# Kernel optimization log

Measured on AMD Instinct MI355X. Metric: run time of the kernel, lower is better.

Reference implementation:

```python
import jax, jax.numpy as jnp
import numpy as np


def dct_matrix(N: int) -> jnp.ndarray:
    # Orthonormal DCT-II matrix: D[k, n] = s_k * cos(pi*(2n+1)k / (2N))
    n = jnp.arange(N, dtype=jnp.float32)
    k = jnp.arange(N, dtype=jnp.float32)[:, None]
    D = jnp.cos(jnp.pi * (2.0 * n + 1.0) * k / (2.0 * N))
    scale = jnp.where(k == 0, jnp.sqrt(1.0 / N), jnp.sqrt(2.0 / N))
    return D * scale


def setup_inputs() -> dict:
    key = jax.random.key(0)
    k1, k2, k3 = jax.random.split(key, 3)
    B, C, H, W = 16, 128, 128, 128
    top_k, red = 16, 4
    x = jax.random.normal(k1, (B, C, H, W), dtype=jnp.float32)
    w1 = jax.random.normal(k2, (top_k, top_k // red), dtype=jnp.float32) * (1.0 / np.sqrt(top_k))
    b1 = jnp.zeros((top_k // red,), dtype=jnp.float32)
    w2 = jax.random.normal(k3, (top_k // red, 1), dtype=jnp.float32) * (1.0 / np.sqrt(top_k // red))
    b2 = jnp.zeros((1,), dtype=jnp.float32)
    return {"x": x, "w1": w1, "b1": b1, "w2": w2, "b2": b2}


def reference(x, w1, b1, w2, b2):
    B, C, H, W = x.shape
    top_k = w1.shape[0]
    # dct_energy uses x.detach() in the original -> no grad through this path
    xs = jax.lax.stop_gradient(x)
    DH = dct_matrix(H)
    DW = dct_matrix(W)
    # 2D orthonormal DCT-II via two matmuls: DH @ x @ DW^T
    t = jnp.einsum('hH,bcHW->bchW', DH, xs)
    dct2 = jnp.einsum('bchW,wW->bchw', t, DW)
    energy = jnp.abs(dct2).mean(axis=1).reshape(B, H * W)  # [B, H*W]
    topk_vals, _ = jax.lax.top_k(energy, top_k)  # [B, top_k], descending
    h = jax.nn.relu(topk_vals @ w1 + b1)
    att = jax.nn.sigmoid(h @ w2 + b2)  # [B, 1]
    return x * att[:, :, None, None]
```

## Files before the change

### kernel.cpp

```cpp
#include <hip/hip_runtime.h>


typedef __attribute__((ext_vector_type(8))) _Float16 half8;
typedef __attribute__((ext_vector_type(16))) float f32x16;

#define NCH 32
#define CPB 4

#define Z16 {0.f,0.f,0.f,0.f,0.f,0.f,0.f,0.f,0.f,0.f,0.f,0.f,0.f,0.f,0.f,0.f}

#define SWZ(row, c) (((((row) * 128 + (c)) * 2)) ^ (((row) & 7) << 4))

__device__ __forceinline__ unsigned short f2h(float f) {
    union { _Float16 h; unsigned short u; } cv;
    cv.h = (_Float16)f;
    return cv.u;
}
__device__ __forceinline__ unsigned int pack2(float a, float b) {
    return (unsigned int)f2h(a) | ((unsigned int)f2h(b) << 16);
}

__global__ __launch_bounds__(256) void dct_prep(unsigned short* __restrict__ Dp) {
    int i = blockIdx.x * 256 + threadIdx.x;
    int j = i & 7, r = (i >> 3) & 127, hi = (i >> 10) & 1, kk = i >> 11;
    int c = kk * 16 + hi * 8 + j;
    float s = (r == 0) ? 0.08838834764831845f : 0.125f;
    float ang = (float)((2 * c + 1) * r) * 0.012271846303085130f;
    Dp[i] = f2h(s * cosf(ang));
}

__global__ __launch_bounds__(512) void dct_energy_kernel(
    const float* __restrict__ x, const unsigned short* __restrict__ Dp,
    float* __restrict__ energy, float* __restrict__ partial)
{
    __shared__ __attribute__((aligned(16))) unsigned short Xs[128 * 128];
    __shared__ __attribute__((aligned(16))) unsigned short Ps[128 * 128];

    const int b = blockIdx.x;
    const int chunk = blockIdx.y;
    const int tid = threadIdx.x;
    const int lane = tid & 63;
    const int wid = tid >> 6;
    const int wm = wid >> 1;
    const int wn = wid & 1;
    const int l31 = lane & 31;
    const int hi = lane >> 5;

    const float4* xb4 = (const float4*)(x + (((size_t)(b * 128 + chunk * CPB)) << 14));

    float en0[16], en1[16];
#pragma unroll
    for (int r = 0; r < 16; ++r) { en0[r] = 0.f; en1[r] = 0.f; }

    const int rowX = 32 * wm + l31;
    const int k2a = 64 * wn + l31;
    const unsigned short* dB0 = Dp + k2a * 8;
    const unsigned short* dB1 = Dp + (k2a + 32) * 8;
    const unsigned short* dA  = Dp + rowX * 8;

    float4 ld[8];
#pragma unroll
    for (int i = 0; i < 8; ++i) ld[i] = xb4[i * 512 + tid];
#pragma unroll
    for (int i = 0; i < 8; ++i) {
        int fidx = i * 512 + tid;
        int row = fidx >> 5, c = (fidx & 31) << 2;
        uint2 v; v.x = pack2(ld[i].x, ld[i].y); v.y = pack2(ld[i].z, ld[i].w);
        *(uint2*)((char*)Xs + SWZ(row, c)) = v;
    }
    __syncthreads();

    for (int s = 0; s < CPB; ++s) {
        if (s + 1 < CPB) {
            const float4* nx = xb4 + ((size_t)(s + 1) << 12);
#pragma unroll
            for (int i = 0; i < 8; ++i) ld[i] = nx[i * 512 + tid];
        }

        f32x16 acc0 = Z16, acc1 = Z16;
#pragma unroll
        for (int kk = 0; kk < 8; ++kk) {
            int c0 = kk * 16 + hi * 8;
            int kb = (kk * 2 + hi) << 10;
            half8 aX = *(const half8*)((const char*)Xs + SWZ(rowX, c0));
            half8 bD0 = *(const half8*)(const void*)(dB0 + kb);
            half8 bD1 = *(const half8*)(const void*)(dB1 + kb);
            acc0 = __builtin_amdgcn_mfma_f32_32x32x16_f16(aX, bD0, acc0, 0, 0, 0);
            acc1 = __builtin_amdgcn_mfma_f32_32x32x16_f16(aX, bD1, acc1, 0, 0, 0);
        }
#pragma unroll
        for (int g = 0; g < 4; ++g) {
            int h0 = 32 * wm + 8 * g + 4 * hi;
            uint2 v0; v0.x = pack2(acc0[4 * g + 0], acc0[4 * g + 1]);
            v0.y = pack2(acc0[4 * g + 2], acc0[4 * g + 3]);
            *(uint2*)((char*)Ps + SWZ(k2a, h0)) = v0;
            uint2 v1; v1.x = pack2(acc1[4 * g + 0], acc1[4 * g + 1]);
            v1.y = pack2(acc1[4 * g + 2], acc1[4 * g + 3]);
            *(uint2*)((char*)Ps + SWZ(k2a + 32, h0)) = v1;
        }
        __syncthreads();

        f32x16 d0 = Z16, d1 = Z16;
#pragma unroll
        for (int kk = 0; kk < 8; ++kk) {
            int c0 = kk * 16 + hi * 8;
            int kb = (kk * 2 + hi) << 10;
            half8 aD = *(const half8*)(const void*)(dA + kb);
            half8 bP0 = *(const half8*)((const char*)Ps + SWZ(k2a, c0));
            half8 bP1 = *(const half8*)((const char*)Ps + SWZ(k2a + 32, c0));
            d0 = __builtin_amdgcn_mfma_f32_32x32x16_f16(aD, bP0, d0, 0, 0, 0);
            d1 = __builtin_amdgcn_mfma_f32_32x32x16_f16(aD, bP1, d1, 0, 0, 0);
        }
#pragma unroll
        for (int r = 0; r < 16; ++r) { en0[r] += fabsf(d0[r]); en1[r] += fabsf(d1[r]); }

        if (s + 1 < CPB) {
#pragma unroll
            for (int i = 0; i < 8; ++i) {
                int fidx = i * 512 + tid;
                int row = fidx >> 5, c = (fidx & 31) << 2;
                uint2 v; v.x = pack2(ld[i].x, ld[i].y); v.y = pack2(ld[i].z, ld[i].w);
                *(uint2*)((char*)Xs + SWZ(row, c)) = v;
            }
        }
        __syncthreads();
    }

    if (partial) {
        float* pb = partial + (((size_t)(b * NCH + chunk)) << 14);
#pragma unroll
        for (int r = 0; r < 16; ++r) {
            int row = 32 * wm + (r & 3) + 8 * (r >> 2) + 4 * hi;
            int idx = row * 128 + k2a;
            pb[idx] = en0[r];
            pb[idx + 32] = en1[r];
        }
    } else {
        float* eb = energy + ((size_t)b << 14);
#pragma unroll
        for (int r = 0; r < 16; ++r) {
            int row = 32 * wm + (r & 3) + 8 * (r >> 2) + 4 * hi;
            int idx = row * 128 + k2a;
            atomicAdd(&eb[idx], en0[r]);
            atomicAdd(&eb[idx + 32], en1[r]);
        }
    }
}

__global__ __launch_bounds__(256) void reduce_energy(
    const float* __restrict__ partial, float* __restrict__ energy)
{
    int g = blockIdx.x * 256 + threadIdx.x;
    int b = g >> 14, i = g & 16383;
    const float* p = partial + (((size_t)b * NCH) << 14) + i;
    float s = 0.f;
#pragma unroll
    for (int ch = 0; ch < NCH; ++ch) s += p[(size_t)ch << 14];
    energy[g] = s;
}

__global__ __launch_bounds__(1024) void topk_mlp(
    const float* __restrict__ energy,
    const float* __restrict__ w1, const float* __restrict__ b1,
    const float* __restrict__ w2, const float* __restrict__ b2,
    float* __restrict__ att)
{
    __shared__ float wv[16];
    __shared__ int   wi[16];
    __shared__ float winv_s;
    __shared__ int   wini_s;
    __shared__ float topv[16];
    int b = blockIdx.x, t = threadIdx.x;
    int lane = t & 63, wid = t >> 6;
    const float* eb = energy + ((size_t)b << 14);

    float v[16];
#pragma unroll
    for (int k = 0; k < 16; ++k) v[k] = eb[k * 1024 + t];
    unsigned mask = 0xFFFFu;

    for (int j = 0; j < 16; ++j) {
        float mv = -1e30f; int mi = 0;
#pragma unroll
        for (int k = 0; k < 16; ++k) {
            if ((mask >> k) & 1u) {
                float c = v[k];
                if (c > mv) { mv = c; mi = k * 1024 + t; }
            }
        }
#pragma unroll
        for (int off = 32; off >= 1; off >>= 1) {
            float ov = __shfl_down(mv, off);
            int   oi = __shfl_down(mi, off);
            if (ov > mv) { mv = ov; mi = oi; }
        }
        if (lane == 0) { wv[wid] = mv; wi[wid] = mi; }
        __syncthreads();
        if (t == 0) {
            float bv = wv[0]; int bi = wi[0];
#pragma unroll
            for (int w = 1; w < 16; ++w)
                if (wv[w] > bv) { bv = wv[w]; bi = wi[w]; }
            winv_s = bv; wini_s = bi;
            topv[j] = bv * (1.0f / 128.0f);
        }
        __syncthreads();
        int gw = wini_s;
        if (t == (gw & 1023)) mask &= ~(1u << (gw >> 10));
    }

    if (t == 0) {
        float z = b2[0];
#pragma unroll
        for (int jj = 0; jj < 4; ++jj) {
            float a = b1[jj];
#pragma unroll
            for (int i = 0; i < 16; ++i) a += topv[i] * w1[i * 4 + jj];
            a = fmaxf(a, 0.0f);
            z += a * w2[jj];
        }
        att[b] = 1.0f / (1.0f + expf(-z));
    }
}

__global__ __launch_bounds__(256) void scale_kernel(
    const float4* __restrict__ x4, const float* __restrict__ att,
    float4* __restrict__ out4, int n4)
{
    int i = blockIdx.x * 256 + threadIdx.x;
    int stride = gridDim.x * 256;
    for (; i < n4; i += stride) {
        float a = att[i >> 19];
        float4 v = x4[i];
        v.x *= a; v.y *= a; v.z *= a; v.w *= a;
        out4[i] = v;
    }
}

extern "C" void kernel_launch(void* const* d_in, const int* in_sizes, int n_in,
                              void* d_out, int out_size, void* d_ws, size_t ws_size,
                              hipStream_t stream) {
    const float* x  = (const float*)d_in[0];
    const float* w1 = (const float*)d_in[1];
    const float* b1 = (const float*)d_in[2];
    const float* w2 = (const float*)d_in[3];
    const float* b2 = (const float*)d_in[4];

    char* wsb = (char*)d_ws;
    unsigned short* Dp = (unsigned short*)wsb;
    float* energy = (float*)(wsb + (1 << 15));
    float* att    = (float*)(wsb + (1 << 15) + (1 << 20));
    float* partial = (float*)(wsb + (1 << 21));
    size_t need_partial = (size_t)(1 << 21) + (size_t)16 * NCH * 16384 * 4;
    bool use_partial = (ws_size >= need_partial);

    dct_prep<<<64, 256, 0, stream>>>(Dp);
    if (!use_partial) hipMemsetAsync(energy, 0, (size_t)16 * 16384 * 4, stream);

    dim3 g2(16, NCH);
    dct_energy_kernel<<<g2, 512, 0, stream>>>(x, Dp, energy,
                                              use_partial ? partial : (float*)nullptr);
    if (use_partial) reduce_energy<<<1024, 256, 0, stream>>>(partial, energy);

    topk_mlp<<<16, 1024, 0, stream>>>(energy, w1, b1, w2, b2, att);
    scale_kernel<<<2048, 256, 0, stream>>>((const float4*)x, att,
                                           (float4*)d_out, out_size / 4);
}
```

Before: 318.3 us.

## Split fused DCT energy kernel into two passes via fp16 intermediate in output buffer

Splits the fused two-stage DCT kernel into two kernels. Pass1 runs one block per (batch, channel) and writes the fp16 row-transformed result to global memory, reusing the output buffer as scratch. Pass2 reads that intermediate directly from global memory for the column transform and accumulates absolute energy across 4 channels per block. This raises parallelism in the first stage (2048 blocks instead of 512) and frees LDS, at the cost of an extra write and read of a 64MB fp16 intermediate.

```diff
diff --git a/kernel.cpp b/kernel.cpp
--- a/kernel.cpp
+++ b/kernel.cpp
@@ -5,7 +5,7 @@
 typedef __attribute__((ext_vector_type(16))) float f32x16;
 
 #define NCH 32
-#define CPB 4
+#define CPB2 4
 
 #define Z16 {0.f,0.f,0.f,0.f,0.f,0.f,0.f,0.f,0.f,0.f,0.f,0.f,0.f,0.f,0.f,0.f}
 
@@ -29,13 +29,78 @@
     Dp[i] = f2h(s * cosf(ang));
 }
 
-__global__ __launch_bounds__(512) void dct_energy_kernel(
+__global__ __launch_bounds__(512) void dct_pass1(
     const float* __restrict__ x, const unsigned short* __restrict__ Dp,
+    unsigned short* __restrict__ PG)
+{
+    __shared__ __attribute__((aligned(16))) unsigned short Xs[128 * 128];
+
+    const int b = blockIdx.x;
+    const int c = blockIdx.y;
+    const int tid = threadIdx.x;
+    const int lane = tid & 63;
+    const int wid = tid >> 6;
+    const int wm = wid >> 1;
+    const int wn = wid & 1;
+    const int l31 = lane & 31;
+    const int hi = lane >> 5;
+
+    const float4* xb4 = (const float4*)(x + (((size_t)(b * 128 + c)) << 14));
+
+#pragma unroll
+    for (int i = 0; i < 8; ++i) {
+        float4 v = xb4[i * 512 + tid];
+        int fidx = i * 512 + tid;
+        int row = fidx >> 5, cc = (fidx & 31) << 2;
+        uint2 u; u.x = pack2(v.x, v.y); u.y = pack2(v.z, v.w);
+        *(uint2*)((char*)Xs + SWZ(row, cc)) = u;
+    }
+    __syncthreads();
+
+    const int rowX = 32 * wm + l31;
+    const int k2a = 64 * wn + l31;
+    const unsigned short* dB0 = Dp + k2a * 8;
+    const unsigned short* dB1 = Dp + (k2a + 32) * 8;
+
+    f32x16 acc0 = Z16, acc1 = Z16;
+#pragma unroll
+    for (int kk = 0; kk < 8; ++kk) {
+        int c0 = kk * 16 + hi * 8;
+        int kb = (kk * 2 + hi) << 10;
+        half8 aX = *(const half8*)((const char*)Xs + SWZ(rowX, c0));
+        half8 bD0 = *(const half8*)(const void*)(dB0 + kb);
+        half8 bD1 = *(const half8*)(const void*)(dB1 + kb);
+        acc0 = __builtin_amdgcn_mfma_f32_32x32x16_f16(aX, bD0, acc0, 0, 0, 0);
+        acc1 = __builtin_amdgcn_mfma_f32_32x32x16_f16(aX, bD1, acc1, 0, 0, 0);
+    }
+    __syncthreads();
+
+#pragma unroll
+    for (int g = 0; g < 4; ++g) {
+        int h0 = 32 * wm + 8 * g + 4 * hi;
+        uint2 v0; v0.x = pack2(acc0[4 * g + 0], acc0[4 * g + 1]);
+        v0.y = pack2(acc0[4 * g + 2], acc0[4 * g + 3]);
+        *(uint2*)((char*)Xs + SWZ(k2a, h0)) = v0;
+        uint2 v1; v1.x = pack2(acc1[4 * g + 0], acc1[4 * g + 1]);
+        v1.y = pack2(acc1[4 * g + 2], acc1[4 * g + 3]);
+        *(uint2*)((char*)Xs + SWZ(k2a + 32, h0)) = v1;
+    }
+    __syncthreads();
+
+    unsigned short* pgs = PG + (((size_t)(b * 128 + c)) << 14);
+#pragma unroll
+    for (int i = 0; i < 4; ++i) {
+        int chunk = i * 512 + tid;
+        int hcg = chunk >> 7, wp = chunk & 127;
+        uint4 v = *(const uint4*)((const char*)Xs + SWZ(wp, hcg * 8));
+        *(uint4*)(pgs + (size_t)chunk * 8) = v;
+    }
+}
+
+__global__ __launch_bounds__(512) void dct_pass2(
+    const unsigned short* __restrict__ PG, const unsigned short* __restrict__ Dp,
     float* __restrict__ energy, float* __restrict__ partial)
 {
-    __shared__ __attribute__((aligned(16))) unsigned short Xs[128 * 128];
-    __shared__ __attribute__((aligned(16))) unsigned short Ps[128 * 128];
-
     const int b = blockIdx.x;
     const int chunk = blockIdx.y;
     const int tid = threadIdx.x;
@@ -46,84 +111,32 @@
     const int l31 = lane & 31;
     const int hi = lane >> 5;
 
-    const float4* xb4 = (const float4*)(x + (((size_t)(b * 128 + chunk * CPB)) << 14));
-
-    float en0[16], en1[16];
-#pragma unroll
-    for (int r = 0; r < 16; ++r) { en0[r] = 0.f; en1[r] = 0.f; }
-
     const int rowX = 32 * wm + l31;
     const int k2a = 64 * wn + l31;
-    const unsigned short* dB0 = Dp + k2a * 8;
-    const unsigned short* dB1 = Dp + (k2a + 32) * 8;
-    const unsigned short* dA  = Dp + rowX * 8;
-
-    float4 ld[8];
-#pragma unroll
-    for (int i = 0; i < 8; ++i) ld[i] = xb4[i * 512 + tid];
-#pragma unroll
-    for (int i = 0; i < 8; ++i) {
-        int fidx = i * 512 + tid;
-        int row = fidx >> 5, c = (fidx & 31) << 2;
-        uint2 v; v.x = pack2(ld[i].x, ld[i].y); v.y = pack2(ld[i].z, ld[i].w);
-        *(uint2*)((char*)Xs + SWZ(row, c)) = v;
-    }
-    __syncthreads();
-
-    for (int s = 0; s < CPB; ++s) {
-        if (s + 1 < CPB) {
-            const float4* nx = xb4 + ((size_t)(s + 1) << 12);
-#pragma unroll
-            for (int i = 0; i < 8; ++i) ld[i] = nx[i * 512 + tid];
-        }
-
-        f32x16 acc0 = Z16, acc1 = Z16;
+    const unsigned short* dA = Dp + rowX * 8;
+
+    float en0[16], en1[16];
+#pragma unroll
+    for (int r = 0; r < 16; ++r) { en0[r] = 0.f; en1[r] = 0.f; }
+
+    for (int s = 0; s < CPB2; ++s) {
+        const unsigned short* pgs =
+            PG + (((size_t)(b * 128 + chunk * CPB2 + s)) << 14);
+        const unsigned short* pB0 = pgs + (size_t)k2a * 8;
+        const unsigned short* pB1 = pB0 + 32 * 8;
+
+        f32x16 d0 = Z16, d1 = Z16;
 #pragma unroll
         for (int kk = 0; kk < 8; ++kk) {
-            int c0 = kk * 16 + hi * 8;
-            int kb = (kk * 2 + hi) << 10;
-            half8 aX = *(const half8*)((const char*)Xs + SWZ(rowX, c0));
-            half8 bD0 = *(const half8*)(const void*)(dB0 + kb);
-            half8 bD1 = *(const half8*)(const void*)(dB1 + kb);
-            acc0 = __builtin_amdgcn_mfma_f32_32x32x16_f16(aX, bD0, acc0, 0, 0, 0);
-            acc1 = __builtin_amdgcn_mfma_f32_32x32x16_f16(aX, bD1, acc1, 0, 0, 0);
-        }
-#pragma unroll
-        for (int g = 0; g < 4; ++g) {
-            int h0 = 32 * wm + 8 * g + 4 * hi;
-            uint2 v0; v0.x = pack2(acc0[4 * g + 0], acc0[4 * g + 1]);
-            v0.y = pack2(acc0[4 * g + 2], acc0[4 * g + 3]);
-            *(uint2*)((char*)Ps + SWZ(k2a, h0)) = v0;
-            uint2 v1; v1.x = pack2(acc1[4 * g + 0], acc1[4 * g + 1]);
-            v1.y = pack2(acc1[4 * g + 2], acc1[4 * g + 3]);
-            *(uint2*)((char*)Ps + SWZ(k2a + 32, h0)) = v1;
-        }
-        __syncthreads();
-
-        f32x16 d0 = Z16, d1 = Z16;
-#pragma unroll
-        for (int kk = 0; kk < 8; ++kk) {
-            int c0 = kk * 16 + hi * 8;
             int kb = (kk * 2 + hi) << 10;
             half8 aD = *(const half8*)(const void*)(dA + kb);
-            half8 bP0 = *(const half8*)((const char*)Ps + SWZ(k2a, c0));
-            half8 bP1 = *(const half8*)((const char*)Ps + SWZ(k2a + 32, c0));
-            d0 = __builtin_amdgcn_mfma_f32_32x32x16_f16(aD, bP0, d0, 0, 0, 0);
-            d1 = __builtin_amdgcn_mfma_f32_32x32x16_f16(aD, bP1, d1, 0, 0, 0);
+            half8 b0 = *(const half8*)(const void*)(pB0 + kb);
+            half8 b1 = *(const half8*)(const void*)(pB1 + kb);
+            d0 = __builtin_amdgcn_mfma_f32_32x32x16_f16(aD, b0, d0, 0, 0, 0);
+            d1 = __builtin_amdgcn_mfma_f32_32x32x16_f16(aD, b1, d1, 0, 0, 0);
         }
 #pragma unroll
         for (int r = 0; r < 16; ++r) { en0[r] += fabsf(d0[r]); en1[r] += fabsf(d1[r]); }
-
-        if (s + 1 < CPB) {
-#pragma unroll
-            for (int i = 0; i < 8; ++i) {
-                int fidx = i * 512 + tid;
-                int row = fidx >> 5, c = (fidx & 31) << 2;
-                uint2 v; v.x = pack2(ld[i].x, ld[i].y); v.y = pack2(ld[i].z, ld[i].w);
-                *(uint2*)((char*)Xs + SWZ(row, c)) = v;
-            }
-        }
-        __syncthreads();
     }
 
     if (partial) {
@@ -254,12 +267,16 @@
     size_t need_partial = (size_t)(1 << 21) + (size_t)16 * NCH * 16384 * 4;
     bool use_partial = (ws_size >= need_partial);
 
+    unsigned short* PG = (unsigned short*)d_out;
+
     dct_prep<<<64, 256, 0, stream>>>(Dp);
     if (!use_partial) hipMemsetAsync(energy, 0, (size_t)16 * 16384 * 4, stream);
 
+    dim3 g1(16, 128);
+    dct_pass1<<<g1, 512, 0, stream>>>(x, Dp, PG);
     dim3 g2(16, NCH);
-    dct_energy_kernel<<<g2, 512, 0, stream>>>(x, Dp, energy,
-                                              use_partial ? partial : (float*)nullptr);
+    dct_pass2<<<g2, 512, 0, stream>>>(PG, Dp, energy,
+                                      use_partial ? partial : (float*)nullptr);
     if (use_partial) reduce_energy<<<1024, 256, 0, stream>>>(partial, energy);
 
     topk_mlp<<<16, 1024, 0, stream>>>(energy, w1, b1, w2, b2, att);
```

Measured after the change: 349.2 us. 1.1x slower.
